# Performance work log

Measured on AMD Instinct MI355X. Metric: run time of the kernel, lower is better.

## Reference

```python
import jax, jax.numpy as jnp
import numpy as np

NUM_EMBEDDINGS = 256
EMBEDDING_DIM = 8


def setup_inputs() -> dict:
    key = jax.random.key(0)
    ks = jax.random.split(key, 8)
    B, D_in, H, D_out = 1024, 512, 2048, 512
    s = lambda fan: 1.0 / np.sqrt(fan)
    return {
        "x": jax.random.normal(ks[0], (B, D_in), dtype=jnp.float32),
        "emb_W": jax.random.normal(ks[1], (NUM_EMBEDDINGS, EMBEDDING_DIM), dtype=jnp.float32),
        "W_in": jax.random.normal(ks[2], (H, D_in), dtype=jnp.float32) * s(D_in),
        "b_in": jax.random.normal(ks[3], (H,), dtype=jnp.float32) * s(D_in),
        "W_h": jax.random.normal(ks[4], (H, H), dtype=jnp.float32) * s(H),
        "b_h": jax.random.normal(ks[5], (H,), dtype=jnp.float32) * s(H),
        "W_out": jax.random.normal(ks[6], (D_out, H), dtype=jnp.float32) * s(H),
        "b_out": jax.random.normal(ks[7], (D_out,), dtype=jnp.float32) * s(H),
    }


def reference(x, emb_W, W_in, b_in, W_h, b_h, W_out, b_out):
    B, D_in = x.shape
    flat = x.reshape(-1)  # [B*D_in], row-major flatten == torch .flatten()
    # power-feature expansion: powers 1..embedding_dim stacked on axis 1
    exps = jnp.arange(1, EMBEDDING_DIM + 1, dtype=x.dtype)
    x_res = flat[:, None] ** exps[None, :]  # [B*D_in, E]
    # get_ind: NOTE source uses sum(flat_x) (not sum of squares) -- faithful
    sm = jnp.sum(x_res, axis=1, keepdims=True)              # [N,1]
    emb = jnp.sum(emb_W * emb_W, axis=1)[None, :]           # [1,K]
    dist = sm + emb - 2.0 * (x_res @ emb_W.T)               # [N,K]
    ind = jnp.argmin(dist, axis=1)                          # [N] int
    # q = ind.view_as(x.T).T : reshape to [D_in, B] then transpose
    q = ind.reshape(D_in, B).T.astype(x.dtype)              # [B, D_in]
    # straight-through: forward value q, gradient flows to x
    q = x + jax.lax.stop_gradient(q - x)
    relu = jax.nn.relu
    h = relu(q @ W_in.T + b_in)      # d_in
    for _ in range(4):               # shared d_h applied 4 times
        h = relu(h @ W_h.T + b_h)
    f = relu(h @ W_out.T + b_out)    # d_out
    q_latent_loss = jnp.float32(0.0)  # eval mode
    return (f, q_latent_loss)
```

## Files before the change

kernel.cpp:

```cpp
#include <hip/hip_runtime.h>
#include <hip/hip_bf16.h>
#include <math.h>


#define B_ROWS 1024
#define D_IN   512
#define HDIM   2048
#define NTOT   (B_ROWS * D_IN)
#define NCODE  256
#define EDIM   8

typedef __attribute__((ext_vector_type(8))) short bf16x8;
typedef __attribute__((ext_vector_type(4))) float f32x4;

__device__ inline void gload_lds16(const void* g, void* l) {
    __builtin_amdgcn_global_load_lds(
        (const __attribute__((address_space(1))) void*)g,
        (__attribute__((address_space(3))) void*)l, 16, 0, 0);
}

__device__ inline ushort bf16_hi_bits(float v, float* hi_f) {
    __hip_bfloat16 h = __float2bfloat16(v);
    *hi_f = __bfloat162float(h);
    ushort u; __builtin_memcpy(&u, &h, 2); return u;
}
__device__ inline ushort bf16_bits(float v) {
    __hip_bfloat16 h = __float2bfloat16(v);
    ushort u; __builtin_memcpy(&u, &h, 2); return u;
}

__global__ __launch_bounds__(256) void fused_pre(
    const float* __restrict__ x, const float* __restrict__ embW,
    const float* __restrict__ Wi, const float* __restrict__ Wh,
    ushort* __restrict__ qhi,
    ushort* __restrict__ wihi, ushort* __restrict__ wilo,
    ushort* __restrict__ whhi, ushort* __restrict__ whlo,
    float* __restrict__ loss_out)
{
    __shared__ float sWE[NCODE][12];
    const int tid = threadIdx.x;

    if (blockIdx.x >= 1024) {
        const int sidx = blockIdx.x - 1024;
        #pragma unroll
        for (int s = 0; s < 4; ++s) {
            const int g = sidx * 1024 + s * 256 + tid;
            const float* src; ushort* hi; ushort* lo; int j;
            if (g < 262144) { src = Wi; hi = wihi; lo = wilo; j = g; }
            else            { src = Wh; hi = whhi; lo = whlo; j = g - 262144; }
            float4 v = reinterpret_cast<const float4*>(src)[j];
            float f[4] = {v.x, v.y, v.z, v.w};
            ushort hh[4], ll[4];
            #pragma unroll
            for (int c = 0; c < 4; ++c) {
                float hf;
                hh[c] = bf16_hi_bits(f[c], &hf);
                ll[c] = bf16_bits(f[c] - hf);
            }
            ushort4 h4 = {hh[0], hh[1], hh[2], hh[3]};
            ushort4 l4 = {ll[0], ll[1], ll[2], ll[3]};
            reinterpret_cast<ushort4*>(hi)[j] = h4;
            reinterpret_cast<ushort4*>(lo)[j] = l4;
        }
        return;
    }

    {
        const float4 a4 = *reinterpret_cast<const float4*>(&embW[tid * EDIM]);
        const float4 b4 = *reinterpret_cast<const float4*>(&embW[tid * EDIM + 4]);
        float s0 = __fmul_rn(a4.x, a4.x), s1 = __fmul_rn(a4.y, a4.y);
        float s2 = __fmul_rn(a4.z, a4.z), s3 = __fmul_rn(a4.w, a4.w);
        float s4 = __fmul_rn(b4.x, b4.x), s5 = __fmul_rn(b4.y, b4.y);
        float s6 = __fmul_rn(b4.z, b4.z), s7 = __fmul_rn(b4.w, b4.w);
        float a = __fadd_rn(__fadd_rn(s0, s1), __fadd_rn(s2, s3));
        float b = __fadd_rn(__fadd_rn(s4, s5), __fadd_rn(s6, s7));
        sWE[tid][0] = a4.x; sWE[tid][1] = a4.y; sWE[tid][2] = a4.z; sWE[tid][3] = a4.w;
        sWE[tid][4] = b4.x; sWE[tid][5] = b4.y; sWE[tid][6] = b4.z; sWE[tid][7] = b4.w;
        sWE[tid][8] = __fadd_rn(a, b);
    }
    __syncthreads();

    const int nbase = blockIdx.x * 512 + tid;

    float p2[2][EDIM], sm[2];
    #pragma unroll
    for (int j = 0; j < 2; ++j) {
        const float v = x[nbase + j * 256];
        float p[EDIM];
        #pragma unroll
        for (int e = 0; e < EDIM; ++e)
            p[e] = powf(v, (float)(e + 1));
        float a = __fadd_rn(__fadd_rn(p[0], p[1]), __fadd_rn(p[2], p[3]));
        float b = __fadd_rn(__fadd_rn(p[4], p[5]), __fadd_rn(p[6], p[7]));
        sm[j] = __fadd_rn(a, b);
        #pragma unroll
        for (int e = 0; e < EDIM; ++e)
            p2[j][e] = 2.0f * p[e];
    }

    float best[2] = {INFINITY, INFINITY};
    int   bi[2]   = {0, 0};
    #pragma unroll 4
    for (int k = 0; k < NCODE; ++k) {
        const float4 w0 = *reinterpret_cast<const float4*>(&sWE[k][0]);
        const float4 w1 = *reinterpret_cast<const float4*>(&sWE[k][4]);
        const float  Ek = sWE[k][8];
        #pragma unroll
        for (int j = 0; j < 2; ++j) {
            float dot = 0.f;
            dot = fmaf(p2[j][0], w0.x, dot); dot = fmaf(p2[j][1], w0.y, dot);
            dot = fmaf(p2[j][2], w0.z, dot); dot = fmaf(p2[j][3], w0.w, dot);
            dot = fmaf(p2[j][4], w1.x, dot); dot = fmaf(p2[j][5], w1.y, dot);
            dot = fmaf(p2[j][6], w1.z, dot); dot = fmaf(p2[j][7], w1.w, dot);
            float d = __fsub_rn(__fadd_rn(sm[j], Ek), dot);
            if (d < best[j]) { best[j] = d; bi[j] = k; }
        }
    }

    #pragma unroll
    for (int j = 0; j < 2; ++j) {
        const int n  = nbase + j * 256;
        const int bo = n & (B_ROWS - 1);
        const int dd = n >> 10;
        qhi[bo * D_IN + dd] = bf16_bits((float)bi[j]);
    }
    if (blockIdx.x == 0 && tid == 0) loss_out[0] = 0.0f;
}

__global__ __launch_bounds__(256) void wo_split(
    const float* __restrict__ Wo, ushort* __restrict__ hi, ushort* __restrict__ lo)
{
    const int tid = threadIdx.x;
    #pragma unroll
    for (int s = 0; s < 4; ++s) {
        const int j = blockIdx.x * 1024 + s * 256 + tid;
        float4 v = reinterpret_cast<const float4*>(Wo)[j];
        float f[4] = {v.x, v.y, v.z, v.w};
        ushort hh[4], ll[4];
        #pragma unroll
        for (int c = 0; c < 4; ++c) {
            float hf;
            hh[c] = bf16_hi_bits(f[c], &hf);
            ll[c] = bf16_bits(f[c] - hf);
        }
        ushort4 h4 = {hh[0], hh[1], hh[2], hh[3]};
        ushort4 l4 = {ll[0], ll[1], ll[2], ll[3]};
        reinterpret_cast<ushort4*>(hi)[j] = h4;
        reinterpret_cast<ushort4*>(lo)[j] = l4;
    }
}

template<bool ALO, bool PARTIAL>
__global__ __launch_bounds__(256) void gemm_split(
    const ushort* __restrict__ Ahi, const ushort* __restrict__ Alo,
    const ushort* __restrict__ Whi, const ushort* __restrict__ Wlo,
    const float* __restrict__ bias,
    ushort* __restrict__ Ohi, ushort* __restrict__ Olo,
    float* __restrict__ OF, int N, int K, int klen)
{
    constexpr int BUF = 49152;
    constexpr int OFF_AH = 0, OFF_AL = 8192, OFF_BH = 16384;
    __shared__ char lds[2 * BUF];

    const int tid = threadIdx.x, lane = tid & 63, wid = tid >> 6;

    const int gy = gridDim.y;
    const int nwg = gridDim.x * gy;
    int lin = blockIdx.x * gy + blockIdx.y;
    int q   = nwg >> 3;
    int sw  = (lin & 7) * q + (lin >> 3);
    int bx  = sw / gy, by2 = sw % gy;
    const int bm   = (by2 & 15) << 6;
    const int kz   = by2 >> 4;
    const int kbeg = kz * klen;
    const int bn   = bx << 7;

    const int wm = (wid >> 1) << 5;
    const int wn = (wid & 1) << 6;

    constexpr int NSEGW = ALO ? 12 : 10;
    const ushort* gp[NSEGW];
    uint ldsoff[NSEGW];
    #pragma unroll
    for (int i = 0; i < NSEGW; ++i) {
        int s = wid + i * 4;
        const ushort* pl; int row0, base, sip;
        if (ALO) {
            if (s < 8)       { pl = Ahi; row0 = bm; base = OFF_AH;         sip = s; }
            else if (s < 16) { pl = Alo; row0 = bm; base = OFF_AL;         sip = s - 8; }
            else if (s < 32) { pl = Whi; row0 = bn; base = OFF_BH;         sip = s - 16; }
            else             { pl = Wlo; row0 = bn; base = OFF_BH + 16384; sip = s - 32; }
        } else {
            if (s < 8)       { pl = Ahi; row0 = bm; base = OFF_AH;         sip = s; }
            else if (s < 24) { pl = Whi; row0 = bn; base = OFF_BH;         sip = s - 8; }
            else             { pl = Wlo; row0 = bn; base = OFF_BH + 16384; sip = s - 24; }
        }
        int r  = sip * 8 + (lane >> 3);
        int ch = (lane & 7) ^ (r & 7);
        gp[i]     = pl + (size_t)(row0 + r) * K + kbeg + ch * 8;
        ldsoff[i] = base + sip * 1024;
    }

    uint aoff[2][2], boff[4][2];
    #pragma unroll
    for (int f = 0; f < 2; ++f) {
        int ar = wm + f * 16 + (lane & 15);
        #pragma unroll
        for (int s = 0; s < 2; ++s) {
            int ch = (s * 4 + (lane >> 4)) ^ (ar & 7);
            aoff[f][s] = OFF_AH + ar * 128 + ch * 16;
        }
    }
    #pragma unroll
    for (int f = 0; f < 4; ++f) {
        int br = wn + f * 16 + (lane & 15);
        #pragma unroll
        for (int s = 0; s < 2; ++s) {
            int ch = (s * 4 + (lane >> 4)) ^ (br & 7);
            boff[f][s] = OFF_BH + br * 128 + ch * 16;
        }
    }

    auto stage = [&](int kt, int b) {
        #pragma unroll
        for (int i = 0; i < NSEGW; ++i)
            gload_lds16(gp[i] + kt * 64, lds + b * BUF + ldsoff[i]);
    };

    f32x4 acc[2][4] = {};
    const int NT = klen >> 6;

    stage(0, 0);
    __syncthreads();

    for (int t = 0; t < NT; ++t) {
        const int cur = t & 1;
        if (t + 1 < NT) stage(t + 1, cur ^ 1);

        const char* lb = lds + cur * BUF;
        bf16x8 aH[2][2], aL[2][2], bH[2][4], bL[2][4];
        #pragma unroll
        for (int s = 0; s < 2; ++s) {
            #pragma unroll
            for (int f = 0; f < 2; ++f) {
                aH[s][f] = *(const bf16x8*)(lb + aoff[f][s]);
                if constexpr (ALO) aL[s][f] = *(const bf16x8*)(lb + aoff[f][s] + 8192);
            }
            #pragma unroll
            for (int f = 0; f < 4; ++f) {
                bH[s][f] = *(const bf16x8*)(lb + boff[f][s]);
                bL[s][f] = *(const bf16x8*)(lb + boff[f][s] + 16384);
            }
        }
        #pragma unroll
        for (int s = 0; s < 2; ++s) {
            #pragma unroll
            for (int fm = 0; fm < 2; ++fm)
                #pragma unroll
                for (int fn = 0; fn < 4; ++fn)
                    acc[fm][fn] = __builtin_amdgcn_mfma_f32_16x16x32_bf16(
                        aH[s][fm], bH[s][fn], acc[fm][fn], 0, 0, 0);
            #pragma unroll
            for (int fm = 0; fm < 2; ++fm)
                #pragma unroll
                for (int fn = 0; fn < 4; ++fn)
                    acc[fm][fn] = __builtin_amdgcn_mfma_f32_16x16x32_bf16(
                        aH[s][fm], bL[s][fn], acc[fm][fn], 0, 0, 0);
            if constexpr (ALO) {
                #pragma unroll
                for (int fm = 0; fm < 2; ++fm)
                    #pragma unroll
                    for (int fn = 0; fn < 4; ++fn)
                        acc[fm][fn] = __builtin_amdgcn_mfma_f32_16x16x32_bf16(
                            aL[s][fm], bH[s][fn], acc[fm][fn], 0, 0, 0);
            }
        }
        __syncthreads();
    }

    #pragma unroll
    for (int fm = 0; fm < 2; ++fm) {
        #pragma unroll
        for (int fn = 0; fn < 4; ++fn) {
            const int col = bn + wn + fn * 16 + (lane & 15);
            const int rb  = bm + wm + fm * 16 + ((lane >> 4) << 2);
            if constexpr (PARTIAL) {
                #pragma unroll
                for (int r = 0; r < 4; ++r)
                    OF[(size_t)(kz * B_ROWS + rb + r) * N + col] = acc[fm][fn][r];
            } else {
                const float bc = bias[col];
                #pragma unroll
                for (int r = 0; r < 4; ++r) {
                    float v = acc[fm][fn][r] + bc;
                    v = v > 0.f ? v : 0.f;
                    float hf;
                    ushort hb = bf16_hi_bits(v, &hf);
                    Ohi[(size_t)(rb + r) * N + col] = hb;
                    Olo[(size_t)(rb + r) * N + col] = bf16_bits(v - hf);
                }
            }
        }
    }
}

__global__ __launch_bounds__(256) void gemm_mid(
    const ushort* __restrict__ Ahi, const ushort* __restrict__ Alo,
    const ushort* __restrict__ Bhi, const ushort* __restrict__ Blo,
    float* __restrict__ OF, int N, int Kfull, int klen)
{
    constexpr int BUF = 65536;
    constexpr int OFF_A[2] = {0, 16384};
    constexpr int OFF_B[2] = {32768, 49152};
    __shared__ char lds[2 * BUF];

    const int tid = threadIdx.x, lane = tid & 63, wid = tid >> 6;

    const int gy = gridDim.y;
    const int nwg = gridDim.x * gy;
    int lin = blockIdx.x * gy + blockIdx.y;
    int q   = nwg >> 3;
    int sw  = (lin & 7) * q + (lin >> 3);
    int bx  = sw / gy, by2 = sw % gy;
    const int bm   = (by2 & 7) << 7;
    const int kz   = by2 >> 3;
    const int kbeg = kz * klen;
    const int bn   = bx << 7;

    const int wm = (wid >> 1) << 6;
    const int wn = (wid & 1) << 6;

    const int ch0 = (lane & 7) ^ (lane >> 3);
    const size_t kstep8 = (size_t)Kfull * 8;
    const ushort* gpb[4];
    uint lob[4];
    {
        const ushort* pls[4] = {Ahi, Alo, Bhi, Blo};
        const int row0s[4]   = {bm, bm, bn, bn};
        const uint bases[4]  = {OFF_A[0], OFF_A[1], OFF_B[0], OFF_B[1]};
        #pragma unroll
        for (int p = 0; p < 4; ++p) {
            gpb[p] = pls[p] + (size_t)(row0s[p] + wid * 32 + (lane >> 3)) * Kfull
                     + kbeg + ch0 * 8;
            lob[p] = bases[p] + wid * 4096;
        }
    }

    uint aoff[4][2], boff[4][2];
    #pragma unroll
    for (int f = 0; f < 4; ++f) {
        #pragma unroll
        for (int ks = 0; ks < 2; ++ks) {
            int ch = (ks * 4 + (lane >> 4)) ^ (lane & 7);
            aoff[f][ks] = OFF_A[0] + (wm + f * 16 + (lane & 15)) * 128 + ch * 16;
            boff[f][ks] = OFF_B[0] + (wn + f * 16 + (lane & 15)) * 128 + ch * 16;
        }
    }

    auto stage = [&](int kt, int b) {
        #pragma unroll
        for (int p = 0; p < 4; ++p)
            #pragma unroll
            for (int i = 0; i < 4; ++i)
                gload_lds16(gpb[p] + i * kstep8 + kt * 64,
                            lds + b * BUF + lob[p] + i * 1024);
    };

    f32x4 acc[4][4] = {};
    const int NT = klen >> 6;

    stage(0, 0);
    __syncthreads();

    for (int t = 0; t < NT; ++t) {
        const int cur = t & 1;
        if (t + 1 < NT) stage(t + 1, cur ^ 1);

        const char* lb = lds + cur * BUF;
        #pragma unroll
        for (int ks = 0; ks < 2; ++ks) {
            bf16x8 aH[4], aL[4], bH[4], bL[4];
            #pragma unroll
            for (int f = 0; f < 4; ++f) {
                aH[f] = *(const bf16x8*)(lb + aoff[f][ks]);
                aL[f] = *(const bf16x8*)(lb + aoff[f][ks] + 16384);
                bH[f] = *(const bf16x8*)(lb + boff[f][ks]);
                bL[f] = *(const bf16x8*)(lb + boff[f][ks] + 16384);
            }
            #pragma unroll
            for (int fm = 0; fm < 4; ++fm)
                #pragma unroll
                for (int fn = 0; fn < 4; ++fn)
                    acc[fm][fn] = __builtin_amdgcn_mfma_f32_16x16x32_bf16(
                        aH[fm], bH[fn], acc[fm][fn], 0, 0, 0);
            #pragma unroll
            for (int fm = 0; fm < 4; ++fm)
                #pragma unroll
                for (int fn = 0; fn < 4; ++fn)
                    acc[fm][fn] = __builtin_amdgcn_mfma_f32_16x16x32_bf16(
                        aH[fm], bL[fn], acc[fm][fn], 0, 0, 0);
            #pragma unroll
            for (int fm = 0; fm < 4; ++fm)
                #pragma unroll
                for (int fn = 0; fn < 4; ++fn)
                    acc[fm][fn] = __builtin_amdgcn_mfma_f32_16x16x32_bf16(
                        aL[fm], bH[fn], acc[fm][fn], 0, 0, 0);
        }
        __syncthreads();
    }

    #pragma unroll
    for (int fm = 0; fm < 4; ++fm) {
        #pragma unroll
        for (int fn = 0; fn < 4; ++fn) {
            const int col = bn + wn + fn * 16 + (lane & 15);
            const int rb  = bm + wm + fm * 16 + ((lane >> 4) << 2);
            #pragma unroll
            for (int r = 0; r < 4; ++r)
                OF[(size_t)(kz * B_ROWS + rb + r) * N + col] = acc[fm][fn][r];
        }
    }
}

__global__ __launch_bounds__(256) void combine_mid(
    const float* __restrict__ part, const float* __restrict__ bias,
    ushort* __restrict__ hi, ushort* __restrict__ lo)
{
    const int i = blockIdx.x * 256 + threadIdx.x;
    const float4* p = (const float4*)part;
    float4 a = p[i], b = p[i + 524288];
    float4 bb = ((const float4*)bias)[i & 511];
    float f[4] = {a.x + b.x + bb.x, a.y + b.y + bb.y,
                  a.z + b.z + bb.z, a.w + b.w + bb.w};
    ushort hh[4], ll[4];
    #pragma unroll
    for (int c = 0; c < 4; ++c) {
        float v = f[c] > 0.f ? f[c] : 0.f;
        float hf;
        hh[c] = bf16_hi_bits(v, &hf);
        ll[c] = bf16_bits(v - hf);
    }
    ushort4 h4 = {hh[0], hh[1], hh[2], hh[3]};
    ushort4 l4 = {ll[0], ll[1], ll[2], ll[3]};
    reinterpret_cast<ushort4*>(hi)[i] = h4;
    reinterpret_cast<ushort4*>(lo)[i] = l4;
}

__global__ __launch_bounds__(256) void combine_relu(
    const float* __restrict__ part, const float* __restrict__ bias,
    float* __restrict__ out)
{
    const int i = blockIdx.x * 256 + threadIdx.x;
    const float4* p = (const float4*)part;
    float4 bb = ((const float4*)bias)[i & 127];
    float ox = bb.x, oy = bb.y, oz = bb.z, ow = bb.w;
    #pragma unroll
    for (int z = 0; z < 8; ++z) {
        float4 a = p[i + z * 131072];
        ox += a.x; oy += a.y; oz += a.z; ow += a.w;
    }
    float4 o;
    o.x = ox > 0.f ? ox : 0.f;
    o.y = oy > 0.f ? oy : 0.f;
    o.z = oz > 0.f ? oz : 0.f;
    o.w = ow > 0.f ? ow : 0.f;
    reinterpret_cast<float4*>(out)[i] = o;
}

extern "C" void kernel_launch(void* const* d_in, const int* in_sizes, int n_in,
                              void* d_out, int out_size, void* d_ws, size_t ws_size,
                              hipStream_t stream)
{
    const float* x     = (const float*)d_in[0];
    const float* emb_W = (const float*)d_in[1];
    const float* W_in  = (const float*)d_in[2];
    const float* b_in  = (const float*)d_in[3];
    const float* W_h   = (const float*)d_in[4];
    const float* b_h   = (const float*)d_in[5];
    const float* W_out = (const float*)d_in[6];
    const float* b_out = (const float*)d_in[7];
    float* out = (float*)d_out;

    char* w = (char*)d_ws;
    const size_t MB = 1 << 20;
    ushort* qhi    = (ushort*)(w);
    ushort* wihi   = (ushort*)(w + 1*MB);
    ushort* wilo   = (ushort*)(w + 3*MB);
    float*  midpar = (float*)(w);
    ushort* wohi   = (ushort*)(w);
    ushort* wolo   = (ushort*)(w + 2*MB);
    ushort* hhi    = (ushort*)(w + 16*MB);
    ushort* hlo    = (ushort*)(w + 20*MB);
    ushort* whhi   = (ushort*)(w + 24*MB);
    ushort* whlo   = (ushort*)(w + 32*MB);
    float*  l6par  = (float*)(w + 24*MB);

    fused_pre<<<2304, 256, 0, stream>>>(x, emb_W, W_in, W_h,
                                        qhi, wihi, wilo, whhi, whlo, out + NTOT);

    gemm_split<false, false><<<dim3(16, 16), 256, 0, stream>>>(
        qhi, nullptr, wihi, wilo, b_in, hhi, hlo, nullptr, HDIM, D_IN, D_IN);

    for (int l = 0; l < 4; ++l) {
        gemm_mid<<<dim3(16, 16), 256, 0, stream>>>(
            hhi, hlo, whhi, whlo, midpar, HDIM, HDIM, 1024);
        combine_mid<<<2048, 256, 0, stream>>>(midpar, b_h, hhi, hlo);
    }

    wo_split<<<256, 256, 0, stream>>>(W_out, wohi, wolo);

    gemm_mid<<<dim3(4, 64), 256, 0, stream>>>(
        hhi, hlo, wohi, wolo, l6par, D_IN, HDIM, 256);

    combine_relu<<<512, 256, 0, stream>>>(l6par, b_out, out);
}
```

Before: 212.2 us.

## Fuse split-K reduction into GEMM epilogue via atomic tile flags; transpose codebook LDS layout

Measured after the change: 350.4 us. 1.65x slower.

```diff
diff --git a/kernel.cpp b/kernel.cpp
--- a/kernel.cpp
+++ b/kernel.cpp
@@ -37,7 +37,7 @@
     ushort* __restrict__ whhi, ushort* __restrict__ whlo,
     float* __restrict__ loss_out)
 {
-    __shared__ float sWE[NCODE][12];
+    __shared__ float sQ[64][40];
     const int tid = threadIdx.x;
 
     if (blockIdx.x >= 1024) {
@@ -66,17 +66,20 @@
     }
 
     {
-        const float4 a4 = *reinterpret_cast<const float4*>(&embW[tid * EDIM]);
-        const float4 b4 = *reinterpret_cast<const float4*>(&embW[tid * EDIM + 4]);
+        const int c = tid, g = c >> 2, u = c & 3;
+        const float4 a4 = *reinterpret_cast<const float4*>(&embW[c * EDIM]);
+        const float4 b4 = *reinterpret_cast<const float4*>(&embW[c * EDIM + 4]);
         float s0 = __fmul_rn(a4.x, a4.x), s1 = __fmul_rn(a4.y, a4.y);
         float s2 = __fmul_rn(a4.z, a4.z), s3 = __fmul_rn(a4.w, a4.w);
         float s4 = __fmul_rn(b4.x, b4.x), s5 = __fmul_rn(b4.y, b4.y);
         float s6 = __fmul_rn(b4.z, b4.z), s7 = __fmul_rn(b4.w, b4.w);
         float a = __fadd_rn(__fadd_rn(s0, s1), __fadd_rn(s2, s3));
         float b = __fadd_rn(__fadd_rn(s4, s5), __fadd_rn(s6, s7));
-        sWE[tid][0] = a4.x; sWE[tid][1] = a4.y; sWE[tid][2] = a4.z; sWE[tid][3] = a4.w;
-        sWE[tid][4] = b4.x; sWE[tid][5] = b4.y; sWE[tid][6] = b4.z; sWE[tid][7] = b4.w;
-        sWE[tid][8] = __fadd_rn(a, b);
+        sQ[g][0 * 4 + u] = a4.x; sQ[g][1 * 4 + u] = a4.y;
+        sQ[g][2 * 4 + u] = a4.z; sQ[g][3 * 4 + u] = a4.w;
+        sQ[g][4 * 4 + u] = b4.x; sQ[g][5 * 4 + u] = b4.y;
+        sQ[g][6 * 4 + u] = b4.z; sQ[g][7 * 4 + u] = b4.w;
+        sQ[g][32 + u]    = __fadd_rn(a, b);
     }
     __syncthreads();
 
@@ -100,20 +103,31 @@
 
     float best[2] = {INFINITY, INFINITY};
     int   bi[2]   = {0, 0};
-    #pragma unroll 4
-    for (int k = 0; k < NCODE; ++k) {
-        const float4 w0 = *reinterpret_cast<const float4*>(&sWE[k][0]);
-        const float4 w1 = *reinterpret_cast<const float4*>(&sWE[k][4]);
-        const float  Ek = sWE[k][8];
-        #pragma unroll
-        for (int j = 0; j < 2; ++j) {
-            float dot = 0.f;
-            dot = fmaf(p2[j][0], w0.x, dot); dot = fmaf(p2[j][1], w0.y, dot);
-            dot = fmaf(p2[j][2], w0.z, dot); dot = fmaf(p2[j][3], w0.w, dot);
-            dot = fmaf(p2[j][4], w1.x, dot); dot = fmaf(p2[j][5], w1.y, dot);
-            dot = fmaf(p2[j][6], w1.z, dot); dot = fmaf(p2[j][7], w1.w, dot);
-            float d = __fsub_rn(__fadd_rn(sm[j], Ek), dot);
-            if (d < best[j]) { best[j] = d; bi[j] = k; }
+
+    #pragma unroll 2
+    for (int g = 0; g < 64; ++g) {
+        const f32x4* q4 = reinterpret_cast<const f32x4*>(sQ[g]);
+        f32x4 ce[9];
+        #pragma unroll
+        for (int e = 0; e < 9; ++e) ce[e] = q4[e];
+        #pragma unroll
+        for (int u = 0; u < 4; ++u) {
+            const int k = g * 4 + u;
+            const float Ek = ce[8][u];
+            #pragma unroll
+            for (int j = 0; j < 2; ++j) {
+                float dot = 0.f;
+                dot = fmaf(p2[j][0], ce[0][u], dot);
+                dot = fmaf(p2[j][1], ce[1][u], dot);
+                dot = fmaf(p2[j][2], ce[2][u], dot);
+                dot = fmaf(p2[j][3], ce[3][u], dot);
+                dot = fmaf(p2[j][4], ce[4][u], dot);
+                dot = fmaf(p2[j][5], ce[5][u], dot);
+                dot = fmaf(p2[j][6], ce[6][u], dot);
+                dot = fmaf(p2[j][7], ce[7][u], dot);
+                float d = __fsub_rn(__fadd_rn(sm[j], Ek), dot);
+                if (d < best[j]) { best[j] = d; bi[j] = k; }
+            }
         }
     }
 
@@ -304,10 +318,14 @@
     }
 }
 
+template<int NSPLIT, bool MID>
 __global__ __launch_bounds__(256) void gemm_mid(
     const ushort* __restrict__ Ahi, const ushort* __restrict__ Alo,
     const ushort* __restrict__ Bhi, const ushort* __restrict__ Blo,
-    float* __restrict__ OF, int N, int Kfull, int klen)
+    float* __restrict__ P, const float* __restrict__ bias,
+    ushort* __restrict__ Ohi, ushort* __restrict__ Olo,
+    float* __restrict__ OUT, uint* __restrict__ flags,
+    int N, int Kfull, int klen)
 {
     constexpr int BUF = 65536;
     constexpr int OFF_A[2] = {0, 16384};
@@ -409,62 +427,110 @@
         __syncthreads();
     }
 
-    #pragma unroll
-    for (int fm = 0; fm < 4; ++fm) {
-        #pragma unroll
-        for (int fn = 0; fn < 4; ++fn) {
-            const int col = bn + wn + fn * 16 + (lane & 15);
-            const int rb  = bm + wm + fm * 16 + ((lane >> 4) << 2);
-            #pragma unroll
-            for (int r = 0; r < 4; ++r)
-                OF[(size_t)(kz * B_ROWS + rb + r) * N + col] = acc[fm][fn][r];
-        }
-    }
-}
-
-__global__ __launch_bounds__(256) void combine_mid(
-    const float* __restrict__ part, const float* __restrict__ bias,
-    ushort* __restrict__ hi, ushort* __restrict__ lo)
-{
-    const int i = blockIdx.x * 256 + threadIdx.x;
-    const float4* p = (const float4*)part;
-    float4 a = p[i], b = p[i + 524288];
-    float4 bb = ((const float4*)bias)[i & 511];
-    float f[4] = {a.x + b.x + bb.x, a.y + b.y + bb.y,
-                  a.z + b.z + bb.z, a.w + b.w + bb.w};
-    ushort hh[4], ll[4];
-    #pragma unroll
-    for (int c = 0; c < 4; ++c) {
-        float v = f[c] > 0.f ? f[c] : 0.f;
-        float hf;
-        hh[c] = bf16_hi_bits(v, &hf);
-        ll[c] = bf16_bits(v - hf);
-    }
-    ushort4 h4 = {hh[0], hh[1], hh[2], hh[3]};
-    ushort4 l4 = {ll[0], ll[1], ll[2], ll[3]};
-    reinterpret_cast<ushort4*>(hi)[i] = h4;
-    reinterpret_cast<ushort4*>(lo)[i] = l4;
-}
-
-__global__ __launch_bounds__(256) void combine_relu(
-    const float* __restrict__ part, const float* __restrict__ bias,
-    float* __restrict__ out)
-{
-    const int i = blockIdx.x * 256 + threadIdx.x;
-    const float4* p = (const float4*)part;
-    float4 bb = ((const float4*)bias)[i & 127];
-    float ox = bb.x, oy = bb.y, oz = bb.z, ow = bb.w;
-    #pragma unroll
-    for (int z = 0; z < 8; ++z) {
-        float4 a = p[i + z * 131072];
-        ox += a.x; oy += a.y; oz += a.z; ow += a.w;
-    }
-    float4 o;
-    o.x = ox > 0.f ? ox : 0.f;
-    o.y = oy > 0.f ? oy : 0.f;
-    o.z = oz > 0.f ? oz : 0.f;
-    o.w = ow > 0.f ? ow : 0.f;
-    reinterpret_cast<float4*>(out)[i] = o;
+    const int tile = bx * 8 + (by2 & 7);
+
+    if constexpr (MID) {
+        __shared__ int role;
+        if (tid == 0) {
+            uint old = __hip_atomic_fetch_add(&flags[tile], 1u,
+                           __ATOMIC_RELAXED, __HIP_MEMORY_SCOPE_AGENT);
+            role = (int)old;
+        }
+        __syncthreads();
+        float* tp = P + (size_t)tile * 16384;
+        if (role == 0) {
+            #pragma unroll
+            for (int fm = 0; fm < 4; ++fm)
+                #pragma unroll
+                for (int fn = 0; fn < 4; ++fn) {
+                    const int lc  = wn + fn * 16 + (lane & 15);
+                    const int lr0 = wm + fm * 16 + ((lane >> 4) << 2);
+                    #pragma unroll
+                    for (int r = 0; r < 4; ++r)
+                        tp[(lr0 + r) * 128 + lc] = acc[fm][fn][r];
+                }
+            __syncthreads();
+            if (tid == 0) {
+                __threadfence();
+                __hip_atomic_store(&flags[128 + tile], 1u,
+                                   __ATOMIC_RELEASE, __HIP_MEMORY_SCOPE_AGENT);
+            }
+            return;
+        }
+        if (tid == 0) {
+            while (__hip_atomic_load(&flags[128 + tile],
+                       __ATOMIC_ACQUIRE, __HIP_MEMORY_SCOPE_AGENT) == 0u)
+                __builtin_amdgcn_s_sleep(2);
+            __threadfence();
+        }
+        __syncthreads();
+        #pragma unroll
+        for (int fm = 0; fm < 4; ++fm)
+            #pragma unroll
+            for (int fn = 0; fn < 4; ++fn) {
+                const int lc  = wn + fn * 16 + (lane & 15);
+                const int gc  = bn + lc;
+                const float bc = bias[gc];
+                const int lr0 = wm + fm * 16 + ((lane >> 4) << 2);
+                #pragma unroll
+                for (int r = 0; r < 4; ++r) {
+                    const float other = tp[(lr0 + r) * 128 + lc];
+                    float v = (kz == 0) ? (acc[fm][fn][r] + other)
+                                        : (other + acc[fm][fn][r]);
+                    v = v + bc;
+                    v = v > 0.f ? v : 0.f;
+                    float hf;
+                    ushort hb = bf16_hi_bits(v, &hf);
+                    const size_t o = (size_t)(bm + lr0 + r) * N + gc;
+                    Ohi[o] = hb;
+                    Olo[o] = bf16_bits(v - hf);
+                }
+            }
+        return;
+    } else {
+        float* tp = P + ((size_t)kz * 32 + tile) * 16384;
+        #pragma unroll
+        for (int fm = 0; fm < 4; ++fm)
+            #pragma unroll
+            for (int fn = 0; fn < 4; ++fn) {
+                const int lc  = wn + fn * 16 + (lane & 15);
+                const int lr0 = wm + fm * 16 + ((lane >> 4) << 2);
+                #pragma unroll
+                for (int r = 0; r < 4; ++r)
+                    tp[(lr0 + r) * 128 + lc] = acc[fm][fn][r];
+            }
+        __shared__ int isLast;
+        __syncthreads();
+        if (tid == 0) {
+            __threadfence();
+            uint old = __hip_atomic_fetch_add(&flags[tile], 1u,
+                           __ATOMIC_ACQ_REL, __HIP_MEMORY_SCOPE_AGENT);
+            isLast = (old == (uint)(NSPLIT - 1));
+            if (isLast) __threadfence();
+        }
+        __syncthreads();
+        if (!isLast) return;
+        for (int i = tid; i < 4096; i += 256) {
+            const int r  = i >> 5;
+            const int c4 = (i & 31) << 2;
+            const int gc = bn + c4;
+            float4 bb = *reinterpret_cast<const float4*>(&bias[gc]);
+            float s0 = bb.x, s1 = bb.y, s2 = bb.z, s3 = bb.w;
+            #pragma unroll
+            for (int z = 0; z < NSPLIT; ++z) {
+                const float4 p = *reinterpret_cast<const float4*>(
+                    P + ((size_t)z * 32 + tile) * 16384 + (size_t)i * 4);
+                s0 += p.x; s1 += p.y; s2 += p.z; s3 += p.w;
+            }
+            float4 o;
+            o.x = s0 > 0.f ? s0 : 0.f;
+            o.y = s1 > 0.f ? s1 : 0.f;
+            o.z = s2 > 0.f ? s2 : 0.f;
+            o.w = s3 > 0.f ? s3 : 0.f;
+            *reinterpret_cast<float4*>(&OUT[(size_t)(bm + r) * N + gc]) = o;
+        }
+        return;
+    }
 }
 
 extern "C" void kernel_launch(void* const* d_in, const int* in_sizes, int n_in,
@@ -483,34 +549,42 @@
 
     char* w = (char*)d_ws;
     const size_t MB = 1 << 20;
-    ushort* qhi    = (ushort*)(w);
-    ushort* wihi   = (ushort*)(w + 1*MB);
-    ushort* wilo   = (ushort*)(w + 3*MB);
-    float*  midpar = (float*)(w);
-    ushort* wohi   = (ushort*)(w);
-    ushort* wolo   = (ushort*)(w + 2*MB);
-    ushort* hhi    = (ushort*)(w + 16*MB);
-    ushort* hlo    = (ushort*)(w + 20*MB);
-    ushort* whhi   = (ushort*)(w + 24*MB);
-    ushort* whlo   = (ushort*)(w + 32*MB);
-    float*  l6par  = (float*)(w + 24*MB);
+    ushort* qhi   = (ushort*)(w);
+    ushort* wihi  = (ushort*)(w + 1*MB);
+    ushort* wilo  = (ushort*)(w + 3*MB);
+    float*  midP  = (float*)(w);
+    ushort* wohi  = (ushort*)(w);
+    ushort* wolo  = (ushort*)(w + 2*MB);
+    ushort* hBhi  = (ushort*)(w + 8*MB);
+    ushort* hBlo  = (ushort*)(w + 12*MB);
+    ushort* hAhi  = (ushort*)(w + 16*MB);
+    ushort* hAlo  = (ushort*)(w + 20*MB);
+    ushort* whhi  = (ushort*)(w + 24*MB);
+    ushort* whlo  = (ushort*)(w + 32*MB);
+    float*  l6par = (float*)(w + 24*MB);
+    uint*   flags = (uint*)(w + 40*MB);
+
+    hipMemsetAsync(flags, 0, 8192, stream);
 
     fused_pre<<<2304, 256, 0, stream>>>(x, emb_W, W_in, W_h,
                                         qhi, wihi, wilo, whhi, whlo, out + NTOT);
 
     gemm_split<false, false><<<dim3(16, 16), 256, 0, stream>>>(
-        qhi, nullptr, wihi, wilo, b_in, hhi, hlo, nullptr, HDIM, D_IN, D_IN);
+        qhi, nullptr, wihi, wilo, b_in, hAhi, hAlo, nullptr, HDIM, D_IN, D_IN);
 
     for (int l = 0; l < 4; ++l) {
-        gemm_mid<<<dim3(16, 16), 256, 0, stream>>>(
-            hhi, hlo, whhi, whlo, midpar, HDIM, HDIM, 1024);
-        combine_mid<<<2048, 256, 0, stream>>>(midpar, b_h, hhi, hlo);
+        const ushort* ihi = (l & 1) ? hBhi : hAhi;
+        const ushort* ilo = (l & 1) ? hBlo : hAlo;
+        ushort* ohi = (l & 1) ? hAhi : hBhi;
+        ushort* olo = (l & 1) ? hAlo : hBlo;
+        gemm_mid<2, true><<<dim3(16, 16), 256, 0, stream>>>(
+            ihi, ilo, whhi, whlo, midP, b_h, ohi, olo, nullptr,
+            flags + l * 256, HDIM, HDIM, 1024);
     }
 
     wo_split<<<256, 256, 0, stream>>>(W_out, wohi, wolo);
 
-    gemm_mid<<<dim3(4, 64), 256, 0, stream>>>(
-        hhi, hlo, wohi, wolo, l6par, D_IN, HDIM, 256);
-
-    combine_relu<<<512, 256, 0, stream>>>(l6par, b_out, out);
-}
+    gemm_mid<8, false><<<dim3(4, 64), 256, 0, stream>>>(
+        hAhi, hAlo, wohi, wolo, l6par, b_out, nullptr, nullptr, out,
+        flags + 1024, D_IN, HDIM, 256);
+}
```
